# Performance work log

Measured on AMD Instinct MI355X. Metric: run time of the kernel, lower is better.

Reference implementation:

```python
import jax, jax.numpy as jnp
import numpy as np

TEMPERATURE = 0.07
B, D = 8192, 256

def _l2norm(x, axis=-1, eps=1e-12):
    # matches torch F.normalize(p=2): x / max(||x||, eps)
    n = jnp.sqrt(jnp.sum(x * x, axis=axis, keepdims=True))
    return x / jnp.maximum(n, eps)

def setup_inputs() -> dict:
    key = jax.random.key(0)
    k1, k2, k3 = jax.random.split(key, 3)
    return {
        "h_emb": jax.random.normal(k1, (B, D), dtype=jnp.float32),
        "r_emb": jax.random.normal(k2, (B, D), dtype=jnp.float32),
        "t_emb": jax.random.normal(k3, (B, D), dtype=jnp.float32),
    }

def reference(h_emb, r_emb, t_emb):
    # query = normalize(h + r); positives/negatives = normalize(t)
    q = _l2norm(h_emb + r_emb, axis=1)          # [B, D]
    t = _l2norm(t_emb, axis=1)                  # [B, D]
    # Dense in-batch similarity. The original builds logits = [pos, off-diag negs];
    # since the diagonal of sim IS the positive similarity, cross-entropy with
    # label 0 equals logsumexp over the full row minus the diagonal entry.
    sim = jnp.einsum('bd,nd->bn', q, t) / TEMPERATURE   # [B, B]
    pos = jnp.diagonal(sim)                              # [B]
    loss = jnp.mean(jax.nn.logsumexp(sim, axis=1) - pos)
    return loss
```

## Files before the change

kernel.cpp:

```cpp
#include <hip/hip_runtime.h>
#include <hip/hip_bf16.h>

#define B_DIM 8192
#define D_DIM 256
#define GRID_GEMM 512
#define NT 16

constexpr float INV_T = 14.285714285714286f;

typedef __bf16 bf16x8 __attribute__((ext_vector_type(8)));
typedef float  f32x16 __attribute__((ext_vector_type(16)));

#define GLOBAL_U32(p) ((const __attribute__((address_space(1))) unsigned int*)(p))
#define LDS_U32(p)    ((__attribute__((address_space(3))) unsigned int*)(p))

#define WAITCNT_VM0 0x0F70

__device__ inline unsigned short f2bf(float f) {
    union { float f; unsigned u; } x; x.f = f;
    unsigned r = x.u + 0x7fffu + ((x.u >> 16) & 1u);
    return (unsigned short)(r >> 16);
}

__global__ __launch_bounds__(256) void norm_kernel(
    const float* __restrict__ h, const float* __restrict__ r,
    const float* __restrict__ t,
    unsigned short* __restrict__ qws, unsigned short* __restrict__ tws,
    float* __restrict__ rowsum, float* __restrict__ diagsum, int* __restrict__ ticket)
{
    if (blockIdx.x == 0) {
        float4* rs4 = (float4*)rowsum;
#pragma unroll
        for (int i = 0; i < 8; ++i)
            rs4[threadIdx.x * 8 + i] = make_float4(0.f, 0.f, 0.f, 0.f);
        if (threadIdx.x == 0) { *diagsum = 0.f; *ticket = 0; }
    }

    const int wave = threadIdx.x >> 6;
    const int lane = threadIdx.x & 63;
    const int wg   = blockIdx.x * 4 + wave;

    const int ks  = lane >> 2;
    const int hi2 = (lane >> 1) & 1;
    const int sub = lane & 1;

#pragma unroll
    for (int i = 0; i < 2; ++i) {
        const int row = wg * 2 + i;
        {
            float4 a = ((const float4*)h)[row * 64 + lane];
            float4 b = ((const float4*)r)[row * 64 + lane];
            float4 v = make_float4(a.x + b.x, a.y + b.y, a.z + b.z, a.w + b.w);
            float s = v.x * v.x + v.y * v.y + v.z * v.z + v.w * v.w;
#pragma unroll
            for (int off = 32; off; off >>= 1) s += __shfl_xor(s, off, 64);
            float scale = INV_T / fmaxf(sqrtf(s), 1e-12f);
            ushort4 o;
            o.x = f2bf(v.x * scale); o.y = f2bf(v.y * scale);
            o.z = f2bf(v.z * scale); o.w = f2bf(v.w * scale);
            size_t slot16 = ((size_t)((row >> 5) * 16 + ks) * 64
                             + (size_t)(hi2 * 32 + (row & 31)));
            *(ushort4*)((unsigned char*)qws + slot16 * 16 + sub * 8) = o;
        }
        {
            float4 v = ((const float4*)t)[row * 64 + lane];
            float s = v.x * v.x + v.y * v.y + v.z * v.z + v.w * v.w;
#pragma unroll
            for (int off = 32; off; off >>= 1) s += __shfl_xor(s, off, 64);
            float scale = 1.0f / fmaxf(sqrtf(s), 1e-12f);
            ushort4 o;
            o.x = f2bf(v.x * scale); o.y = f2bf(v.y * scale);
            o.z = f2bf(v.z * scale); o.w = f2bf(v.w * scale);
            size_t slot16 = ((size_t)((row >> 5) * 16 + ks) * 64
                             + (size_t)(hi2 * 32 + (row & 31)));
            *(ushort4*)((unsigned char*)tws + slot16 * 16 + sub * 8) = o;
        }
    }
}

__global__ __launch_bounds__(256, 2) void gemm_lse_kernel(
    const unsigned char* __restrict__ qws, const unsigned char* __restrict__ tws,
    float* __restrict__ rowsum, float* __restrict__ diagsum,
    int* __restrict__ ticket, float* __restrict__ out)
{
    __shared__ __align__(16) unsigned char ldsB[4][32 * 512];
    __shared__ float wred[4];
    __shared__ int lastflag;

    const int tid  = threadIdx.x;
    const int lane = tid & 63;
    const int w    = tid >> 6;
    const int l31  = lane & 31;
    const int hi   = lane >> 5;

    const int cc   = blockIdx.x & 15;
    const int rb   = blockIdx.x >> 4;
    const int row0 = rb * 256 + w * 64;
    const int col0 = cc * 512;
    const int tile0 = cc * 16;

#define STAGE(st, bufi)                                                      \
    {                                                                        \
        const unsigned char* gs = tws + (size_t)(tile0 + (st)) * 16384;      \
        _Pragma("unroll")                                                    \
        for (int it = 0; it < 4; ++it)                                       \
            __builtin_amdgcn_global_load_lds(                                \
                GLOBAL_U32(gs + (it * 256 + tid) * 16),                      \
                LDS_U32(&ldsB[bufi][(it * 256 + tid) * 16]), 16, 0, 0);      \
    }

    STAGE(0, 0);
    STAGE(1, 1);

    bf16x8 a[2][16];
    {
        const unsigned char* abase = qws + (size_t)row0 * 512 + lane * 16;
#pragma unroll
        for (int rt = 0; rt < 2; ++rt)
#pragma unroll
            for (int ks = 0; ks < 16; ++ks)
                a[rt][ks] = *(const bf16x8*)(abase + rt * 16384 + ks * 1024);
    }

    f32x16 rowacc[2] = {};
    float diagacc = 0.f;

#define PROCESS_TILE(t)                                                      \
    {                                                                        \
        const unsigned char* bbuf = ldsB[(t) & 3] + lane * 16;               \
        f32x16 acc0 = {}, acc1 = {};                                         \
        _Pragma("unroll")                                                    \
        for (int ks = 0; ks < 16; ++ks) {                                    \
            bf16x8 b = *(const bf16x8*)(bbuf + ks * 1024);                   \
            acc0 = __builtin_amdgcn_mfma_f32_32x32x16_bf16(a[0][ks], b, acc0, 0, 0, 0); \
            acc1 = __builtin_amdgcn_mfma_f32_32x32x16_bf16(a[1][ks], b, acc1, 0, 0, 0); \
        }                                                                    \
        _Pragma("unroll")                                                    \
        for (int g = 0; g < 16; ++g) {                                       \
            rowacc[0][g] += __expf(acc0[g] - INV_T);                         \
            rowacc[1][g] += __expf(acc1[g] - INV_T);                         \
        }                                                                    \
        const int c0t = col0 + (t) * 32;                                     \
        if (c0t == row0) {                                                   \
            _Pragma("unroll")                                                \
            for (int g = 0; g < 16; ++g) {                                   \
                int rm = (g & 3) + 8 * (g >> 2) + 4 * hi;                    \
                if (l31 == rm) diagacc += acc0[g];                           \
            }                                                                \
        }                                                                    \
        if (c0t == row0 + 32) {                                              \
            _Pragma("unroll")                                                \
            for (int g = 0; g < 16; ++g) {                                   \
                int rm = (g & 3) + 8 * (g >> 2) + 4 * hi;                    \
                if (l31 == rm) diagacc += acc1[g];                           \
            }                                                                \
        }                                                                    \
    }

    for (int r = 0; r < 8; ++r) {
        __builtin_amdgcn_s_waitcnt(WAITCNT_VM0);
        __builtin_amdgcn_s_barrier();
        if (r < 7) {
            STAGE(2 * r + 2, (2 * r + 2) & 3);
            STAGE(2 * r + 3, (2 * r + 3) & 3);
        }
        PROCESS_TILE(2 * r);
        PROCESS_TILE(2 * r + 1);
    }

#pragma unroll
    for (int rt = 0; rt < 2; ++rt)
#pragma unroll
        for (int g = 0; g < 16; ++g) {
            float s = rowacc[rt][g];
            s += __shfl_xor(s, 1, 64);
            s += __shfl_xor(s, 2, 64);
            s += __shfl_xor(s, 4, 64);
            s += __shfl_xor(s, 8, 64);
            s += __shfl_xor(s, 16, 64);
            if (l31 == 0) {
                int grow = row0 + rt * 32 + (g & 3) + 8 * (g >> 2) + 4 * hi;
                atomicAdd(&rowsum[grow], s);
            }
        }

    float dsum = diagacc;
#pragma unroll
    for (int off = 32; off; off >>= 1) dsum += __shfl_xor(dsum, off, 64);
    if (lane == 0 && dsum != 0.f) atomicAdd(diagsum, dsum);

    __syncthreads();
    if (tid == 0) {
        __threadfence();
        int old = __hip_atomic_fetch_add(ticket, 1, __ATOMIC_ACQ_REL,
                                         __HIP_MEMORY_SCOPE_AGENT);
        lastflag = (old == GRID_GEMM - 1);
    }
    __syncthreads();
    if (!lastflag) return;

    float lsum = 0.f;
    for (int rr = tid; rr < B_DIM; rr += 256) {
        float rs = __hip_atomic_load(&rowsum[rr], __ATOMIC_RELAXED,
                                     __HIP_MEMORY_SCOPE_AGENT);
        lsum += __logf(rs);
    }
#pragma unroll
    for (int off = 32; off; off >>= 1) lsum += __shfl_xor(lsum, off, 64);
    if (lane == 0) wred[w] = lsum;
    __syncthreads();
    if (tid == 0) {
        float ds = __hip_atomic_load(diagsum, __ATOMIC_RELAXED,
                                     __HIP_MEMORY_SCOPE_AGENT);
        float total = wred[0] + wred[1] + wred[2] + wred[3]
                    + (float)B_DIM * INV_T
                    - ds;
        out[0] = total / (float)B_DIM;
    }
}

extern "C" void kernel_launch(void* const* d_in, const int* in_sizes, int n_in,
                              void* d_out, int out_size, void* d_ws, size_t ws_size,
                              hipStream_t stream)
{
    const float* h = (const float*)d_in[0];
    const float* r = (const float*)d_in[1];
    const float* t = (const float*)d_in[2];

    unsigned char* ws = (unsigned char*)d_ws;
    unsigned short* qws = (unsigned short*)ws;
    unsigned short* tws = (unsigned short*)(ws + 4u * 1024 * 1024);
    float* rowsum  = (float*)(ws + 8u * 1024 * 1024);
    float* diagsum = (float*)(ws + 8u * 1024 * 1024 + 32u * 1024);
    int*   ticket  = (int*)  (ws + 8u * 1024 * 1024 + 32u * 1024 + 16);

    norm_kernel<<<1024, 256, 0, stream>>>(h, r, t, qws, tws, rowsum, diagsum, ticket);
    gemm_lse_kernel<<<GRID_GEMM, 256, 0, stream>>>(
        (const unsigned char*)qws, (const unsigned char*)tws,
        rowsum, diagsum, ticket, (float*)d_out);
}
```

Measured before the change: 132.0 us.

## Switch GEMM from 32x32x16 to 16x16x32 bf16 MFMA with matching layout

Replaces the 32x32x16 MFMA tiling with 16x16x32 bf16 MFMAs, so each wave computes four 16-row blocks against two 16-column halves of each 32-column tile. The normalization kernel writes a new swizzled workspace layout to match the 16x16 operand format, and the diagonal extraction and row-sum reduction are rewritten for the 16x16 accumulator lane mapping. The aim is better MFMA throughput and scheduling, and a shorter shuffle reduction. The cost is more MFMA instructions and more accumulator bookkeeping per tile.

```diff
diff --git a/kernel.cpp b/kernel.cpp
--- a/kernel.cpp
+++ b/kernel.cpp
@@ -9,7 +9,7 @@
 constexpr float INV_T = 14.285714285714286f;
 
 typedef __bf16 bf16x8 __attribute__((ext_vector_type(8)));
-typedef float  f32x16 __attribute__((ext_vector_type(16)));
+typedef float  f32x4  __attribute__((ext_vector_type(4)));
 
 #define GLOBAL_U32(p) ((const __attribute__((address_space(1))) unsigned int*)(p))
 #define LDS_U32(p)    ((__attribute__((address_space(3))) unsigned int*)(p))
@@ -40,9 +40,9 @@
     const int lane = threadIdx.x & 63;
     const int wg   = blockIdx.x * 4 + wave;
 
-    const int ks  = lane >> 2;
-    const int hi2 = (lane >> 1) & 1;
-    const int sub = lane & 1;
+    const int kst  = lane >> 3;
+    const int krun = (lane >> 1) & 3;
+    const int sub8 = lane & 1;
 
 #pragma unroll
     for (int i = 0; i < 2; ++i) {
@@ -58,9 +58,9 @@
             ushort4 o;
             o.x = f2bf(v.x * scale); o.y = f2bf(v.y * scale);
             o.z = f2bf(v.z * scale); o.w = f2bf(v.w * scale);
-            size_t slot16 = ((size_t)((row >> 5) * 16 + ks) * 64
-                             + (size_t)(hi2 * 32 + (row & 31)));
-            *(ushort4*)((unsigned char*)qws + slot16 * 16 + sub * 8) = o;
+            size_t slot16 = ((size_t)((row >> 4) * 8 + kst) * 64
+                             + (size_t)(krun * 16 + (row & 15)));
+            *(ushort4*)((unsigned char*)qws + slot16 * 16 + sub8 * 8) = o;
         }
         {
             float4 v = ((const float4*)t)[row * 64 + lane];
@@ -71,9 +71,9 @@
             ushort4 o;
             o.x = f2bf(v.x * scale); o.y = f2bf(v.y * scale);
             o.z = f2bf(v.z * scale); o.w = f2bf(v.w * scale);
-            size_t slot16 = ((size_t)((row >> 5) * 16 + ks) * 64
-                             + (size_t)(hi2 * 32 + (row & 31)));
-            *(ushort4*)((unsigned char*)tws + slot16 * 16 + sub * 8) = o;
+            size_t slot16 = ((size_t)((row >> 4) * 8 + kst) * 64
+                             + (size_t)(krun * 16 + (row & 15)));
+            *(ushort4*)((unsigned char*)tws + slot16 * 16 + sub8 * 8) = o;
         }
     }
 }
@@ -90,8 +90,8 @@
     const int tid  = threadIdx.x;
     const int lane = tid & 63;
     const int w    = tid >> 6;
-    const int l31  = lane & 31;
-    const int hi   = lane >> 5;
+    const int l15  = lane & 15;
+    const int hi4  = lane >> 4;
 
     const int cc   = blockIdx.x & 15;
     const int rb   = blockIdx.x >> 4;
@@ -112,48 +112,53 @@
     STAGE(0, 0);
     STAGE(1, 1);
 
-    bf16x8 a[2][16];
+    bf16x8 a[4][8];
     {
         const unsigned char* abase = qws + (size_t)row0 * 512 + lane * 16;
 #pragma unroll
-        for (int rt = 0; rt < 2; ++rt)
-#pragma unroll
-            for (int ks = 0; ks < 16; ++ks)
-                a[rt][ks] = *(const bf16x8*)(abase + rt * 16384 + ks * 1024);
-    }
-
-    f32x16 rowacc[2] = {};
+        for (int r = 0; r < 4; ++r)
+#pragma unroll
+            for (int kst = 0; kst < 8; ++kst)
+                a[r][kst] = *(const bf16x8*)(abase + r * 8192 + kst * 1024);
+    }
+
+    float rowacc[16] = {};
     float diagacc = 0.f;
 
 #define PROCESS_TILE(t)                                                      \
     {                                                                        \
         const unsigned char* bbuf = ldsB[(t) & 3] + lane * 16;               \
-        f32x16 acc0 = {}, acc1 = {};                                         \
+        f32x4 acc[4][2] = {};                                                \
         _Pragma("unroll")                                                    \
-        for (int ks = 0; ks < 16; ++ks) {                                    \
-            bf16x8 b = *(const bf16x8*)(bbuf + ks * 1024);                   \
-            acc0 = __builtin_amdgcn_mfma_f32_32x32x16_bf16(a[0][ks], b, acc0, 0, 0, 0); \
-            acc1 = __builtin_amdgcn_mfma_f32_32x32x16_bf16(a[1][ks], b, acc1, 0, 0, 0); \
+        for (int kst = 0; kst < 8; ++kst) {                                  \
+            bf16x8 b0 = *(const bf16x8*)(bbuf + kst * 1024);                 \
+            bf16x8 b1 = *(const bf16x8*)(bbuf + 8192 + kst * 1024);          \
+            _Pragma("unroll")                                                \
+            for (int r = 0; r < 4; ++r) {                                    \
+                acc[r][0] = __builtin_amdgcn_mfma_f32_16x16x32_bf16(         \
+                                a[r][kst], b0, acc[r][0], 0, 0, 0);          \
+                acc[r][1] = __builtin_amdgcn_mfma_f32_16x16x32_bf16(         \
+                                a[r][kst], b1, acc[r][1], 0, 0, 0);          \
+            }                                                                \
         }                                                                    \
         _Pragma("unroll")                                                    \
-        for (int g = 0; g < 16; ++g) {                                       \
-            rowacc[0][g] += __expf(acc0[g] - INV_T);                         \
-            rowacc[1][g] += __expf(acc1[g] - INV_T);                         \
-        }                                                                    \
+        for (int r = 0; r < 4; ++r)                                          \
+            _Pragma("unroll")                                                \
+            for (int g = 0; g < 4; ++g)                                      \
+                rowacc[r * 4 + g] += __expf(acc[r][0][g] - INV_T)            \
+                                   + __expf(acc[r][1][g] - INV_T);           \
         const int c0t = col0 + (t) * 32;                                     \
         if (c0t == row0) {                                                   \
             _Pragma("unroll")                                                \
-            for (int g = 0; g < 16; ++g) {                                   \
-                int rm = (g & 3) + 8 * (g >> 2) + 4 * hi;                    \
-                if (l31 == rm) diagacc += acc0[g];                           \
-            }                                                                \
+            for (int g = 0; g < 4; ++g)                                      \
+                if (l15 == hi4 * 4 + g)                                      \
+                    diagacc += acc[0][0][g] + acc[1][1][g];                  \
         }                                                                    \
         if (c0t == row0 + 32) {                                              \
             _Pragma("unroll")                                                \
-            for (int g = 0; g < 16; ++g) {                                   \
-                int rm = (g & 3) + 8 * (g >> 2) + 4 * hi;                    \
-                if (l31 == rm) diagacc += acc1[g];                           \
-            }                                                                \
+            for (int g = 0; g < 4; ++g)                                      \
+                if (l15 == hi4 * 4 + g)                                      \
+                    diagacc += acc[2][0][g] + acc[3][1][g];                  \
         }                                                                    \
     }
 
@@ -169,20 +174,17 @@
     }
 
 #pragma unroll
-    for (int rt = 0; rt < 2; ++rt)
-#pragma unroll
-        for (int g = 0; g < 16; ++g) {
-            float s = rowacc[rt][g];
-            s += __shfl_xor(s, 1, 64);
-            s += __shfl_xor(s, 2, 64);
-            s += __shfl_xor(s, 4, 64);
-            s += __shfl_xor(s, 8, 64);
-            s += __shfl_xor(s, 16, 64);
-            if (l31 == 0) {
-                int grow = row0 + rt * 32 + (g & 3) + 8 * (g >> 2) + 4 * hi;
-                atomicAdd(&rowsum[grow], s);
-            }
-        }
+    for (int rr = 0; rr < 16; ++rr) {
+        float s = rowacc[rr];
+        s += __shfl_xor(s, 1, 64);
+        s += __shfl_xor(s, 2, 64);
+        s += __shfl_xor(s, 4, 64);
+        s += __shfl_xor(s, 8, 64);
+        if (l15 == 0) {
+            int grow = row0 + (rr >> 2) * 16 + hi4 * 4 + (rr & 3);
+            atomicAdd(&rowsum[grow], s);
+        }
+    }
 
     float dsum = diagacc;
 #pragma unroll
```

Result: faster. 125.5 us (-4.9%).
